# Kernel tuning notes

Measured on AMD Instinct MI355X. Metric: run time of the kernel, lower is better.

Reference implementation:

```python
import jax, jax.numpy as jnp
import numpy as np

B, A, N_OBS, HX, N_ACT = 8192, 32, 128, 64, 16

def setup_inputs() -> dict:
    key = jax.random.key(0)
    ks = jax.random.split(key, 12)
    s = lambda *shape: 0.05 * jax.random.normal(ks[setup_inputs.i], shape, dtype=jnp.float32)
    out = {}
    setup_inputs.i = 0
    def nxt(*shape):
        setup_inputs.i += 1
        return 0.05 * jax.random.normal(ks[setup_inputs.i], shape, dtype=jnp.float32)
    out['obs'] = jax.random.normal(ks[0], (B, A, N_OBS), dtype=jnp.float32)
    out['W1'] = nxt(A, N_OBS, 128); out['b1'] = nxt(A, 128)
    out['W2'] = nxt(A, 128, HX);   out['b2'] = nxt(A, HX)
    out['Wg'] = nxt(A, HX, 2);     out['bg'] = nxt(A, 2)
    out['Wc'] = nxt(A, 2 * HX, HX); out['bc'] = nxt(A, HX)
    out['Wd'] = nxt(A, HX, N_ACT); out['bd'] = nxt(A, N_ACT)
    out['comm_mask'] = jax.random.randint(jax.random.fold_in(key, 99), (A, A), 0, 2, dtype=jnp.int32)
    return out

def reference(obs, W1, b1, W2, b2, Wg, bg, Wc, bc, Wd, bd, comm_mask):
    # encode: per-agent 2-layer MLP, batched over agents via einsum
    x = jax.nn.relu(jnp.einsum('ban,anh->bah', obs, W1) + b1)      # [B,A,128]
    h = jax.nn.relu(jnp.einsum('bah,ahk->bak', x, W2) + b2)        # [B,A,HX]
    # gate: Linear->ReLU->Softmax (computed as in original; only used via the
    # host-side RNG in the torch code, externalized here as comm_mask)
    gates = jax.nn.softmax(jax.nn.relu(jnp.einsum('bak,akg->bag', h, Wg) + bg), axis=-1)
    # communication: for agent i, mean of hidden states of communicating j != i
    mask = comm_mask.astype(h.dtype) * (1.0 - jnp.eye(A, dtype=h.dtype))  # [A_i, A_j]
    total = jnp.einsum('ij,bjk->bik', mask, h)                      # [B,A,HX]
    count = mask.sum(axis=1)                                        # [A]
    comm = total / jnp.maximum(count, 1.0)[None, :, None]           # count==0 -> zeros
    comm_in = jnp.concatenate([h, comm], axis=-1)                   # [B,A,2*HX]
    h2 = jnp.tanh(jnp.einsum('bac,ack->bak', comm_in, Wc) + bc)     # [B,A,HX]
    q = jnp.einsum('bak,akn->ban', h2, Wd) + bd                     # [B,A,N_ACT]
    return q
```

## Files before the change

kernel.cpp:

```cpp
#include <hip/hip_runtime.h>


#define NB   8192
#define NA   32
#define NOBS 128
#define NH1  128
#define HXX  64
#define NACT 16

typedef _Float16 half8  __attribute__((ext_vector_type(8)));
typedef _Float16 half2v __attribute__((ext_vector_type(2)));
typedef float    floatx4 __attribute__((ext_vector_type(4)));

#define MFMA16(af, bf, c) __builtin_amdgcn_mfma_f32_16x16x32_f16((af), (bf), (c), 0, 0, 0)

#define HWS_OFF 0
#define W1P_OFF (NB * NA * HXX)
#define W1P_CNT (NA * 8 * 4 * 512)
#define W2P_OFF (W1P_OFF + W1P_CNT)
#define W2P_CNT (NA * 4 * 4 * 512)
#define WCP_OFF (W2P_OFF + W2P_CNT)
#define WCP_CNT (NA * 4 * 4 * 512)
#define WDP_OFF (WCP_OFF + WCP_CNT)
#define WDP_CNT (NA * 1 * 2 * 512)

#define DEC_LDS (512 * 136 * 2 + 32 * 32 * 4 + 32 * 4)

extern "C" __global__ void pack_kernel(const float* __restrict__ src,
                                       _Float16* __restrict__ dst,
                                       int K, int N, int NT, int NS, int total)
{
    int e = blockIdx.x * 256 + threadIdx.x;
    if (e >= total) return;
    int j = e & 7, l = (e >> 3) & 63;
    int rest = e >> 9;
    int s  = rest % NS; rest /= NS;
    int nt = rest % NT; rest /= NT;
    int a  = rest;
    int k = s * 32 + (l >> 4) * 8 + j;
    int n = nt * 16 + (l & 15);
    dst[e] = (_Float16)src[((size_t)a * K + k) * N + n];
}

extern "C" __global__ __launch_bounds__(256)
void enc_kernel(const float* __restrict__ obs,
                const float* __restrict__ b1,
                const float* __restrict__ b2,
                const _Float16* __restrict__ W1p,
                const _Float16* __restrict__ W2p,
                _Float16* __restrict__ hws)
{
    __shared__ _Float16 A[128 * 136];

    const int t  = threadIdx.x;
    const int a  = blockIdx.y;
    const int b0 = blockIdx.x * 128;

    {
        const int r = t >> 1, hh = t & 1;
        const float4* src = (const float4*)(obs + ((size_t)(b0 + r) * NA + a) * NOBS) + hh * 16;
        _Float16* dst = A + r * 136 + hh * 64;
        #pragma unroll
        for (int q = 0; q < 16; ++q) {
            float4 g = src[q];
            dst[q * 4 + 0] = (_Float16)g.x; dst[q * 4 + 1] = (_Float16)g.y;
            dst[q * 4 + 2] = (_Float16)g.z; dst[q * 4 + 3] = (_Float16)g.w;
        }
    }
    const int w = t >> 6, l = t & 63, lm = l & 15, lq = l >> 4;

    float b1v[8], b2v[4];
    #pragma unroll
    for (int nt = 0; nt < 8; ++nt) b1v[nt] = b1[a * NH1 + nt * 16 + lm];
    #pragma unroll
    for (int nt = 0; nt < 4; ++nt) b2v[nt] = b2[a * HXX + nt * 16 + lm];

    __syncthreads();

    floatx4 acc[2][8];
    #pragma unroll
    for (int mt = 0; mt < 2; ++mt)
        #pragma unroll
        for (int nt = 0; nt < 8; ++nt) acc[mt][nt] = (floatx4){0.f, 0.f, 0.f, 0.f};

    for (int s = 0; s < 4; ++s) {
        half8 af[2];
        #pragma unroll
        for (int mt = 0; mt < 2; ++mt)
            af[mt] = *(const half8*)&A[(w * 32 + mt * 16 + lm) * 136 + s * 32 + lq * 8];
        #pragma unroll
        for (int nt = 0; nt < 8; ++nt) {
            half8 bf = *(const half8*)&W1p[(((a * 8 + nt) * 4 + s) * 512) + l * 8];
            acc[0][nt] = MFMA16(af[0], bf, acc[0][nt]);
            acc[1][nt] = MFMA16(af[1], bf, acc[1][nt]);
        }
    }

    #pragma unroll
    for (int mt = 0; mt < 2; ++mt)
        #pragma unroll
        for (int nt = 0; nt < 8; ++nt)
            #pragma unroll
            for (int v = 0; v < 4; ++v) {
                float x = fmaxf(acc[mt][nt][v] + b1v[nt], 0.f);
                A[(w * 32 + mt * 16 + lq * 4 + v) * 136 + nt * 16 + lm] = (_Float16)x;
            }

    floatx4 acc2[2][4];
    #pragma unroll
    for (int mt = 0; mt < 2; ++mt)
        #pragma unroll
        for (int nt = 0; nt < 4; ++nt) acc2[mt][nt] = (floatx4){0.f, 0.f, 0.f, 0.f};

    for (int s = 0; s < 4; ++s) {
        half8 af[2];
        #pragma unroll
        for (int mt = 0; mt < 2; ++mt)
            af[mt] = *(const half8*)&A[(w * 32 + mt * 16 + lm) * 136 + s * 32 + lq * 8];
        #pragma unroll
        for (int nt = 0; nt < 4; ++nt) {
            half8 bf = *(const half8*)&W2p[(((a * 4 + nt) * 4 + s) * 512) + l * 8];
            acc2[0][nt] = MFMA16(af[0], bf, acc2[0][nt]);
            acc2[1][nt] = MFMA16(af[1], bf, acc2[1][nt]);
        }
    }

    #pragma unroll
    for (int mt = 0; mt < 2; ++mt)
        #pragma unroll
        for (int nt = 0; nt < 4; ++nt)
            #pragma unroll
            for (int v = 0; v < 4; ++v) {
                float x = fmaxf(acc2[mt][nt][v] + b2v[nt], 0.f);
                int row = w * 32 + mt * 16 + lq * 4 + v;
                hws[((size_t)(b0 + row) * NA + a) * HXX + nt * 16 + lm] = (_Float16)x;
            }
}

extern "C" __global__ __launch_bounds__(512)
void dec_kernel(const _Float16* __restrict__ hws,
                const int* __restrict__ cmask,
                const float* __restrict__ bc,
                const float* __restrict__ bd,
                const _Float16* __restrict__ Wcp,
                const _Float16* __restrict__ Wdp,
                float* __restrict__ out)
{
    extern __shared__ char smem[];
    _Float16* A  = (_Float16*)smem;
    float*    Mn = (float*)(smem + 512 * 136 * 2);
    int*      cnt = (int*)(Mn + 32 * 32);

    const int t  = threadIdx.x;
    const int b0 = blockIdx.x * 16;

    {
        const uint4* src = (const uint4*)(hws + (size_t)b0 * NA * HXX);
        #pragma unroll
        for (int it = 0; it < 8; ++it) {
            int idx = it * 512 + t;
            int r = idx >> 8, rem = idx & 255;
            int i = rem >> 3, c8 = rem & 7;
            *(uint4*)&A[(i * 16 + r) * 136 + c8 * 8] = src[idx];
        }
    }
    if (t < NA) {
        int c = 0;
        for (int j = 0; j < NA; ++j) c += (j != t && cmask[t * NA + j]) ? 1 : 0;
        cnt[t] = c;
    }
    __syncthreads();

    for (int e = t; e < NA * NA; e += 512) {
        int i = e >> 5, j = e & 31;
        float v = 0.f;
        if (j != i && cmask[i * NA + j]) {
            int c = cnt[i]; v = 1.0f / (float)(c > 1 ? c : 1);
        }
        Mn[e] = v;
    }
    __syncthreads();

    {
        const int r = t >> 5, cw = t & 31;
        float h0[32], h1[32];
        #pragma unroll
        for (int j = 0; j < 32; ++j) {
            half2v hp = *(const half2v*)&A[(j * 16 + r) * 136 + cw * 2];
            h0[j] = (float)hp[0]; h1[j] = (float)hp[1];
        }
        for (int i = 0; i < 32; ++i) {
            const float4* mr = (const float4*)&Mn[i * 32];
            float a0 = 0.f, a1 = 0.f;
            #pragma unroll
            for (int j4 = 0; j4 < 8; ++j4) {
                float4 m = mr[j4];
                a0 += m.x * h0[j4*4+0] + m.y * h0[j4*4+1] + m.z * h0[j4*4+2] + m.w * h0[j4*4+3];
                a1 += m.x * h1[j4*4+0] + m.y * h1[j4*4+1] + m.z * h1[j4*4+2] + m.w * h1[j4*4+3];
            }
            half2v o; o[0] = (_Float16)a0; o[1] = (_Float16)a1;
            *(half2v*)&A[(i * 16 + r) * 136 + 64 + cw * 2] = o;
        }
    }
    __syncthreads();

    const int w = t >> 6, l = t & 63, lm = l & 15, lq = l >> 4;

    floatx4 acc[4][4];
    #pragma unroll
    for (int g = 0; g < 4; ++g)
        #pragma unroll
        for (int nt = 0; nt < 4; ++nt) acc[g][nt] = (floatx4){0.f, 0.f, 0.f, 0.f};

    for (int s = 0; s < 4; ++s) {
        #pragma unroll
        for (int g = 0; g < 4; ++g) {
            int ag = w * 4 + g;
            half8 af = *(const half8*)&A[(ag * 16 + lm) * 136 + s * 32 + lq * 8];
            #pragma unroll
            for (int nt = 0; nt < 4; ++nt) {
                half8 bf = *(const half8*)&Wcp[(((ag * 4 + nt) * 4 + s) * 512) + l * 8];
                acc[g][nt] = MFMA16(af, bf, acc[g][nt]);
            }
        }
    }
    __syncthreads();

    #pragma unroll
    for (int g = 0; g < 4; ++g) {
        int ag = w * 4 + g;
        #pragma unroll
        for (int nt = 0; nt < 4; ++nt) {
            float bcv = bc[ag * HXX + nt * 16 + lm];
            #pragma unroll
            for (int v = 0; v < 4; ++v) {
                float x = tanhf(acc[g][nt][v] + bcv);
                A[(ag * 16 + lq * 4 + v) * 72 + nt * 16 + lm] = (_Float16)x;
            }
        }
    }

    floatx4 acc3[4];
    #pragma unroll
    for (int g = 0; g < 4; ++g) acc3[g] = (floatx4){0.f, 0.f, 0.f, 0.f};

    for (int s = 0; s < 2; ++s) {
        #pragma unroll
        for (int g = 0; g < 4; ++g) {
            int ag = w * 4 + g;
            half8 af = *(const half8*)&A[(ag * 16 + lm) * 72 + s * 32 + lq * 8];
            half8 bf = *(const half8*)&Wdp[((ag * 2 + s) * 512) + l * 8];
            acc3[g] = MFMA16(af, bf, acc3[g]);
        }
    }

    #pragma unroll
    for (int g = 0; g < 4; ++g) {
        int ag = w * 4 + g;
        float bdv = bd[ag * NACT + lm];
        #pragma unroll
        for (int v = 0; v < 4; ++v) {
            int row = lq * 4 + v;
            out[((size_t)(b0 + row) * NA + ag) * NACT + lm] = acc3[g][v] + bdv;
        }
    }
}

extern "C" void kernel_launch(void* const* d_in, const int* in_sizes, int n_in,
                              void* d_out, int out_size, void* d_ws, size_t ws_size,
                              hipStream_t stream)
{
    const float* obs = (const float*)d_in[0];
    const float* W1  = (const float*)d_in[1];
    const float* b1  = (const float*)d_in[2];
    const float* W2  = (const float*)d_in[3];
    const float* b2  = (const float*)d_in[4];
    const float* Wc  = (const float*)d_in[7];
    const float* bc  = (const float*)d_in[8];
    const float* Wd  = (const float*)d_in[9];
    const float* bd  = (const float*)d_in[10];
    const int*   cm  = (const int*)d_in[11];

    float*    outp = (float*)d_out;
    _Float16* ws   = (_Float16*)d_ws;

    _Float16* hws = ws + HWS_OFF;
    _Float16* W1p = ws + W1P_OFF;
    _Float16* W2p = ws + W2P_OFF;
    _Float16* Wcp = ws + WCP_OFF;
    _Float16* Wdp = ws + WDP_OFF;

    hipLaunchKernelGGL(pack_kernel, dim3(W1P_CNT / 256), dim3(256), 0, stream,
                       W1, W1p, 128, 128, 8, 4, W1P_CNT);
    hipLaunchKernelGGL(pack_kernel, dim3(W2P_CNT / 256), dim3(256), 0, stream,
                       W2, W2p, 128, 64, 4, 4, W2P_CNT);
    hipLaunchKernelGGL(pack_kernel, dim3(WCP_CNT / 256), dim3(256), 0, stream,
                       Wc, Wcp, 128, 64, 4, 4, WCP_CNT);
    hipLaunchKernelGGL(pack_kernel, dim3(WDP_CNT / 256), dim3(256), 0, stream,
                       Wd, Wdp, 64, 16, 1, 2, WDP_CNT);

    hipLaunchKernelGGL(enc_kernel, dim3(NB / 128, NA), dim3(256), 0, stream,
                       obs, b1, b2, W1p, W2p, hws);

    (void)hipFuncSetAttribute((const void*)dec_kernel,
                              hipFuncAttributeMaxDynamicSharedMemorySize, DEC_LDS);
    hipLaunchKernelGGL(dec_kernel, dim3(NB / 16), dim3(512), DEC_LDS, stream,
                       hws, cm, bc, bd, Wcp, Wdp, outp);
}
```

Measured before the change: 326.7 us.

## Merge pack launches, shrink encoder/decoder tiles, coalesce stores, use fast tanh

Merges the four weight-pack launches into one kernel. The encoder block shrinks from 128 to 64 rows, with one M-tile per wave, vectorized half4 conversion stores, and the h output staged through LDS so global writes are 16-byte. The decoder handles 8 batch rows per block instead of 16 to cut LDS use and raise occupancy, duplicating rows inside the 16-row MFMA tile so half of each MFMA is wasted work. It also replaces tanhf with an exp-based fast tanh, drops a barrier, and simplifies the comm reduction to one column per thread.

```diff
diff --git a/kernel.cpp b/kernel.cpp
--- a/kernel.cpp
+++ b/kernel.cpp
@@ -8,8 +8,8 @@
 #define HXX  64
 #define NACT 16
 
-typedef _Float16 half8  __attribute__((ext_vector_type(8)));
-typedef _Float16 half2v __attribute__((ext_vector_type(2)));
+typedef _Float16 half8 __attribute__((ext_vector_type(8)));
+typedef _Float16 half4 __attribute__((ext_vector_type(4)));
 typedef float    floatx4 __attribute__((ext_vector_type(4)));
 
 #define MFMA16(af, bf, c) __builtin_amdgcn_mfma_f32_16x16x32_f16((af), (bf), (c), 0, 0, 0)
@@ -23,26 +23,45 @@
 #define WCP_CNT (NA * 4 * 4 * 512)
 #define WDP_OFF (WCP_OFF + WCP_CNT)
 #define WDP_CNT (NA * 1 * 2 * 512)
-
-#define DEC_LDS (512 * 136 * 2 + 32 * 32 * 4 + 32 * 4)
-
-extern "C" __global__ void pack_kernel(const float* __restrict__ src,
-                                       _Float16* __restrict__ dst,
-                                       int K, int N, int NT, int NS, int total)
+#define PACK_TOTAL (W1P_CNT + W2P_CNT + WCP_CNT + WDP_CNT)
+
+#define DEC_LDS (256 * 136 * 2 + 32 * 32 * 4 + 128)
+
+__device__ __forceinline__ float fast_tanh(float x) {
+    x = fminf(fmaxf(x, -10.f), 10.f);
+    float e2 = __expf(2.f * x);
+    return (e2 - 1.f) / (e2 + 1.f);
+}
+
+extern "C" __global__ void pack_kernel(const float* __restrict__ W1,
+                                       const float* __restrict__ W2,
+                                       const float* __restrict__ Wc,
+                                       const float* __restrict__ Wd,
+                                       _Float16* __restrict__ ws)
 {
     int e = blockIdx.x * 256 + threadIdx.x;
-    if (e >= total) return;
-    int j = e & 7, l = (e >> 3) & 63;
-    int rest = e >> 9;
+    if (e >= PACK_TOTAL) return;
+    const float* src; _Float16* dst; int K, N, NT, NS, r;
+    if (e < W1P_CNT) {
+        src = W1; dst = ws + W1P_OFF; K = 128; N = 128; NT = 8; NS = 4; r = e;
+    } else if (e < W1P_CNT + W2P_CNT) {
+        src = W2; dst = ws + W2P_OFF; K = 128; N = 64; NT = 4; NS = 4; r = e - W1P_CNT;
+    } else if (e < W1P_CNT + W2P_CNT + WCP_CNT) {
+        src = Wc; dst = ws + WCP_OFF; K = 128; N = 64; NT = 4; NS = 4; r = e - W1P_CNT - W2P_CNT;
+    } else {
+        src = Wd; dst = ws + WDP_OFF; K = 64; N = 16; NT = 1; NS = 2; r = e - W1P_CNT - W2P_CNT - WCP_CNT;
+    }
+    int j = r & 7, l = (r >> 3) & 63;
+    int rest = r >> 9;
     int s  = rest % NS; rest /= NS;
     int nt = rest % NT; rest /= NT;
     int a  = rest;
     int k = s * 32 + (l >> 4) * 8 + j;
     int n = nt * 16 + (l & 15);
-    dst[e] = (_Float16)src[((size_t)a * K + k) * N + n];
-}
-
-extern "C" __global__ __launch_bounds__(256)
+    dst[r] = (_Float16)src[((size_t)a * K + k) * N + n];
+}
+
+extern "C" __global__ __launch_bounds__(256, 8)
 void enc_kernel(const float* __restrict__ obs,
                 const float* __restrict__ b1,
                 const float* __restrict__ b2,
@@ -50,21 +69,26 @@
                 const _Float16* __restrict__ W2p,
                 _Float16* __restrict__ hws)
 {
-    __shared__ _Float16 A[128 * 136];
+    __shared__ _Float16 A[64 * 136];
 
     const int t  = threadIdx.x;
     const int a  = blockIdx.y;
-    const int b0 = blockIdx.x * 128;
+    const int b0 = blockIdx.x * 64;
 
     {
-        const int r = t >> 1, hh = t & 1;
-        const float4* src = (const float4*)(obs + ((size_t)(b0 + r) * NA + a) * NOBS) + hh * 16;
-        _Float16* dst = A + r * 136 + hh * 64;
-        #pragma unroll
-        for (int q = 0; q < 16; ++q) {
-            float4 g = src[q];
-            dst[q * 4 + 0] = (_Float16)g.x; dst[q * 4 + 1] = (_Float16)g.y;
-            dst[q * 4 + 2] = (_Float16)g.z; dst[q * 4 + 3] = (_Float16)g.w;
+        const int j = t & 7;
+        #pragma unroll
+        for (int p = 0; p < 2; ++p) {
+            const int row = (t >> 3) + 32 * p;
+            const float4* src = (const float4*)(obs + ((size_t)(b0 + row) * NA + a) * NOBS);
+            _Float16* dst = A + row * 136;
+            #pragma unroll
+            for (int q = 0; q < 4; ++q) {
+                float4 g = src[j + 8 * q];
+                half4 hv; hv[0] = (_Float16)g.x; hv[1] = (_Float16)g.y;
+                hv[2] = (_Float16)g.z; hv[3] = (_Float16)g.w;
+                *(half4*)&dst[(j + 8 * q) * 4] = hv;
+            }
         }
     }
     const int w = t >> 6, l = t & 63, lm = l & 15, lq = l >> 4;
@@ -77,67 +101,55 @@
 
     __syncthreads();
 
-    floatx4 acc[2][8];
-    #pragma unroll
-    for (int mt = 0; mt < 2; ++mt)
-        #pragma unroll
-        for (int nt = 0; nt < 8; ++nt) acc[mt][nt] = (floatx4){0.f, 0.f, 0.f, 0.f};
-
+    floatx4 acc[8];
+    #pragma unroll
+    for (int nt = 0; nt < 8; ++nt) acc[nt] = (floatx4){0.f, 0.f, 0.f, 0.f};
     for (int s = 0; s < 4; ++s) {
-        half8 af[2];
-        #pragma unroll
-        for (int mt = 0; mt < 2; ++mt)
-            af[mt] = *(const half8*)&A[(w * 32 + mt * 16 + lm) * 136 + s * 32 + lq * 8];
+        half8 af = *(const half8*)&A[(w * 16 + lm) * 136 + s * 32 + lq * 8];
         #pragma unroll
         for (int nt = 0; nt < 8; ++nt) {
             half8 bf = *(const half8*)&W1p[(((a * 8 + nt) * 4 + s) * 512) + l * 8];
-            acc[0][nt] = MFMA16(af[0], bf, acc[0][nt]);
-            acc[1][nt] = MFMA16(af[1], bf, acc[1][nt]);
-        }
-    }
-
-    #pragma unroll
-    for (int mt = 0; mt < 2; ++mt)
-        #pragma unroll
-        for (int nt = 0; nt < 8; ++nt)
-            #pragma unroll
-            for (int v = 0; v < 4; ++v) {
-                float x = fmaxf(acc[mt][nt][v] + b1v[nt], 0.f);
-                A[(w * 32 + mt * 16 + lq * 4 + v) * 136 + nt * 16 + lm] = (_Float16)x;
-            }
-
-    floatx4 acc2[2][4];
-    #pragma unroll
-    for (int mt = 0; mt < 2; ++mt)
-        #pragma unroll
-        for (int nt = 0; nt < 4; ++nt) acc2[mt][nt] = (floatx4){0.f, 0.f, 0.f, 0.f};
-
+            acc[nt] = MFMA16(af, bf, acc[nt]);
+        }
+    }
+    #pragma unroll
+    for (int nt = 0; nt < 8; ++nt)
+        #pragma unroll
+        for (int v = 0; v < 4; ++v) {
+            float x = fmaxf(acc[nt][v] + b1v[nt], 0.f);
+            A[(w * 16 + lq * 4 + v) * 136 + nt * 16 + lm] = (_Float16)x;
+        }
+
+    floatx4 acc2[4];
+    #pragma unroll
+    for (int nt = 0; nt < 4; ++nt) acc2[nt] = (floatx4){0.f, 0.f, 0.f, 0.f};
     for (int s = 0; s < 4; ++s) {
-        half8 af[2];
-        #pragma unroll
-        for (int mt = 0; mt < 2; ++mt)
-            af[mt] = *(const half8*)&A[(w * 32 + mt * 16 + lm) * 136 + s * 32 + lq * 8];
+        half8 af = *(const half8*)&A[(w * 16 + lm) * 136 + s * 32 + lq * 8];
         #pragma unroll
         for (int nt = 0; nt < 4; ++nt) {
             half8 bf = *(const half8*)&W2p[(((a * 4 + nt) * 4 + s) * 512) + l * 8];
-            acc2[0][nt] = MFMA16(af[0], bf, acc2[0][nt]);
-            acc2[1][nt] = MFMA16(af[1], bf, acc2[1][nt]);
-        }
-    }
-
-    #pragma unroll
-    for (int mt = 0; mt < 2; ++mt)
-        #pragma unroll
-        for (int nt = 0; nt < 4; ++nt)
-            #pragma unroll
-            for (int v = 0; v < 4; ++v) {
-                float x = fmaxf(acc2[mt][nt][v] + b2v[nt], 0.f);
-                int row = w * 32 + mt * 16 + lq * 4 + v;
-                hws[((size_t)(b0 + row) * NA + a) * HXX + nt * 16 + lm] = (_Float16)x;
-            }
-}
-
-extern "C" __global__ __launch_bounds__(512)
+            acc2[nt] = MFMA16(af, bf, acc2[nt]);
+        }
+    }
+    #pragma unroll
+    for (int nt = 0; nt < 4; ++nt)
+        #pragma unroll
+        for (int v = 0; v < 4; ++v) {
+            float x = fmaxf(acc2[nt][v] + b2v[nt], 0.f);
+            A[(w * 16 + lq * 4 + v) * 136 + nt * 16 + lm] = (_Float16)x;
+        }
+    {
+        const int rr = l >> 2, cc = l & 3;
+        #pragma unroll
+        for (int hh = 0; hh < 2; ++hh) {
+            const int chunk = cc + 4 * hh;
+            half8 hv = *(const half8*)&A[(w * 16 + rr) * 136 + chunk * 8];
+            *(half8*)&hws[((size_t)(b0 + w * 16 + rr) * NA + a) * HXX + chunk * 8] = hv;
+        }
+    }
+}
+
+extern "C" __global__ __launch_bounds__(512, 4)
 void dec_kernel(const _Float16* __restrict__ hws,
                 const int* __restrict__ cmask,
                 const float* __restrict__ bc,
@@ -147,21 +159,20 @@
                 float* __restrict__ out)
 {
     extern __shared__ char smem[];
-    _Float16* A  = (_Float16*)smem;
-    float*    Mn = (float*)(smem + 512 * 136 * 2);
-    int*      cnt = (int*)(Mn + 32 * 32);
+    _Float16* H  = (_Float16*)smem;
+    float*    Mn = (float*)(smem + 256 * 136 * 2);
+    int*      cnt = (int*)(Mn + 1024);
 
     const int t  = threadIdx.x;
-    const int b0 = blockIdx.x * 16;
+    const int b0 = blockIdx.x * 8;
 
     {
         const uint4* src = (const uint4*)(hws + (size_t)b0 * NA * HXX);
         #pragma unroll
-        for (int it = 0; it < 8; ++it) {
+        for (int it = 0; it < 4; ++it) {
             int idx = it * 512 + t;
-            int r = idx >> 8, rem = idx & 255;
-            int i = rem >> 3, c8 = rem & 7;
-            *(uint4*)&A[(i * 16 + r) * 136 + c8 * 8] = src[idx];
+            int r = idx >> 8, rem = idx & 255, ai = rem >> 3, c8 = rem & 7;
+            *(uint4*)&H[(ai * 8 + r) * 136 + c8 * 8] = src[idx];
         }
     }
     if (t < NA) {
@@ -182,29 +193,21 @@
     __syncthreads();
 
     {
-        const int r = t >> 5, cw = t & 31;
-        float h0[32], h1[32];
-        #pragma unroll
-        for (int j = 0; j < 32; ++j) {
-            half2v hp = *(const half2v*)&A[(j * 16 + r) * 136 + cw * 2];
-            h0[j] = (float)hp[0]; h1[j] = (float)hp[1];
-        }
-        for (int i = 0; i < 32; ++i) {
-            const float4* mr = (const float4*)&Mn[i * 32];
-            float a0 = 0.f, a1 = 0.f;
+        const int r = t >> 6, cw = t & 63;
+        float hj[NA];
+        #pragma unroll
+        for (int j = 0; j < NA; ++j) hj[j] = (float)H[(j * 8 + r) * 136 + cw];
+        for (int i = 0; i < NA; ++i) {
+            float acc = 0.f;
             #pragma unroll
-            for (int j4 = 0; j4 < 8; ++j4) {
-                float4 m = mr[j4];
-                a0 += m.x * h0[j4*4+0] + m.y * h0[j4*4+1] + m.z * h0[j4*4+2] + m.w * h0[j4*4+3];
-                a1 += m.x * h1[j4*4+0] + m.y * h1[j4*4+1] + m.z * h1[j4*4+2] + m.w * h1[j4*4+3];
-            }
-            half2v o; o[0] = (_Float16)a0; o[1] = (_Float16)a1;
-            *(half2v*)&A[(i * 16 + r) * 136 + 64 + cw * 2] = o;
+            for (int j = 0; j < NA; ++j) acc += Mn[i * 32 + j] * hj[j];
+            H[(i * 8 + r) * 136 + 64 + cw] = (_Float16)acc;
         }
     }
     __syncthreads();
 
     const int w = t >> 6, l = t & 63, lm = l & 15, lq = l >> 4;
+    const int rdup = lm & 7;
 
     floatx4 acc[4][4];
     #pragma unroll
@@ -216,7 +219,7 @@
         #pragma unroll
         for (int g = 0; g < 4; ++g) {
             int ag = w * 4 + g;
-            half8 af = *(const half8*)&A[(ag * 16 + lm) * 136 + s * 32 + lq * 8];
+            half8 af = *(const half8*)&H[(ag * 8 + rdup) * 136 + s * 32 + lq * 8];
             #pragma unroll
             for (int nt = 0; nt < 4; ++nt) {
                 half8 bf = *(const half8*)&Wcp[(((ag * 4 + nt) * 4 + s) * 512) + l * 8];
@@ -224,7 +227,6 @@
             }
         }
     }
-    __syncthreads();
 
     #pragma unroll
     for (int g = 0; g < 4; ++g) {
@@ -232,10 +234,13 @@
         #pragma unroll
         for (int nt = 0; nt < 4; ++nt) {
             float bcv = bc[ag * HXX + nt * 16 + lm];
-            #pragma unroll
-            for (int v = 0; v < 4; ++v) {
-                float x = tanhf(acc[g][nt][v] + bcv);
-                A[(ag * 16 + lq * 4 + v) * 72 + nt * 16 + lm] = (_Float16)x;
+            if (lq < 2) {
+                #pragma unroll
+                for (int v = 0; v < 4; ++v) {
+                    int m = lq * 4 + v;
+                    float x = fast_tanh(acc[g][nt][v] + bcv);
+                    H[(ag * 8 + m) * 136 + nt * 16 + lm] = (_Float16)x;
+                }
             }
         }
     }
@@ -243,12 +248,11 @@
     floatx4 acc3[4];
     #pragma unroll
     for (int g = 0; g < 4; ++g) acc3[g] = (floatx4){0.f, 0.f, 0.f, 0.f};
-
     for (int s = 0; s < 2; ++s) {
         #pragma unroll
         for (int g = 0; g < 4; ++g) {
             int ag = w * 4 + g;
-            half8 af = *(const half8*)&A[(ag * 16 + lm) * 72 + s * 32 + lq * 8];
+            half8 af = *(const half8*)&H[(ag * 8 + rdup) * 136 + s * 32 + lq * 8];
             half8 bf = *(const half8*)&Wdp[((ag * 2 + s) * 512) + l * 8];
             acc3[g] = MFMA16(af, bf, acc3[g]);
         }
@@ -258,10 +262,12 @@
     for (int g = 0; g < 4; ++g) {
         int ag = w * 4 + g;
         float bdv = bd[ag * NACT + lm];
-        #pragma unroll
-        for (int v = 0; v < 4; ++v) {
-            int row = lq * 4 + v;
-            out[((size_t)(b0 + row) * NA + ag) * NACT + lm] = acc3[g][v] + bdv;
+        if (lq < 2) {
+            #pragma unroll
+            for (int v = 0; v < 4; ++v) {
+                int m = lq * 4 + v;
+                out[((size_t)(b0 + m) * NA + ag) * NACT + lm] = acc3[g][v] + bdv;
+            }
         }
     }
 }
@@ -290,20 +296,14 @@
     _Float16* Wcp = ws + WCP_OFF;
     _Float16* Wdp = ws + WDP_OFF;
 
-    hipLaunchKernelGGL(pack_kernel, dim3(W1P_CNT / 256), dim3(256), 0, stream,
-                       W1, W1p, 128, 128, 8, 4, W1P_CNT);
-    hipLaunchKernelGGL(pack_kernel, dim3(W2P_CNT / 256), dim3(256), 0, stream,
-                       W2, W2p, 128, 64, 4, 4, W2P_CNT);
-    hipLaunchKernelGGL(pack_kernel, dim3(WCP_CNT / 256), dim3(256), 0, stream,
-                       Wc, Wcp, 128, 64, 4, 4, WCP_CNT);
-    hipLaunchKernelGGL(pack_kernel, dim3(WDP_CNT / 256), dim3(256), 0, stream,
-                       Wd, Wdp, 64, 16, 1, 2, WDP_CNT);
-
-    hipLaunchKernelGGL(enc_kernel, dim3(NB / 128, NA), dim3(256), 0, stream,
+    hipLaunchKernelGGL(pack_kernel, dim3((PACK_TOTAL + 255) / 256), dim3(256), 0, stream,
+                       W1, W2, Wc, Wd, ws);
+
+    hipLaunchKernelGGL(enc_kernel, dim3(NB / 64, NA), dim3(256), 0, stream,
                        obs, b1, b2, W1p, W2p, hws);
 
     (void)hipFuncSetAttribute((const void*)dec_kernel,
                               hipFuncAttributeMaxDynamicSharedMemorySize, DEC_LDS);
-    hipLaunchKernelGGL(dec_kernel, dim3(NB / 16), dim3(512), DEC_LDS, stream,
+    hipLaunchKernelGGL(dec_kernel, dim3(NB / 8), dim3(512), DEC_LDS, stream,
                        hws, cm, bc, bd, Wcp, Wdp, outp);
 }
```

New measurement: 355.8 us. 8.9% more time.
